# Optimization experiments

Hardware: AMD Instinct MI355X
Metric: run time of the kernel (lower is better)

Reference implementation:

```python
import jax, jax.numpy as jnp
import numpy as np
from jax import lax

B, CIN, H, W = 8, 3, 512, 512
NF, NDOWN, FEAT = 16, 4, 3
NUM_IDS = 32
EPS = 1e-5
DN = ('NCHW', 'OIHW', 'NCHW')


def _inorm(x):
    # torch InstanceNorm2d(affine=False): per-sample per-channel, biased var, eps=1e-5
    m = jnp.mean(x, axis=(2, 3), keepdims=True)
    v = jnp.var(x, axis=(2, 3), keepdims=True)
    return (x - m) * lax.rsqrt(v + EPS)


def _conv(x, w, b, stride=1, pad=0):
    y = lax.conv_general_dilated(x, w, (stride, stride), ((pad, pad), (pad, pad)), dimension_numbers=DN)
    return y + b[None, :, None, None]


def _tconv(x, w, b):
    # torch ConvTranspose2d(k=3, s=2, p=1, output_padding=1); w in torch layout (Cin, Cout, 3, 3)
    wk = jnp.flip(jnp.transpose(w, (1, 0, 2, 3)), axis=(2, 3))  # -> OIHW
    y = lax.conv_general_dilated(x, wk, (1, 1), ((1, 2), (1, 2)), lhs_dilation=(2, 2), dimension_numbers=DN)
    return y + b[None, :, None, None]


def _rpad(x, p):
    return jnp.pad(x, ((0, 0), (0, 0), (p, p), (p, p)), mode='reflect')


def _forward(x, instance_map, w_in, b_in, wd, bd, wu, bu, w_out, b_out):
    h = jax.nn.relu(_inorm(_conv(_rpad(x, 3), w_in, b_in)))
    for w_, b_ in zip(wd, bd):
        h = jax.nn.relu(_inorm(_conv(h, w_, b_, stride=2, pad=1)))
    for w_, b_ in zip(wu, bu):
        h = jax.nn.relu(_inorm(_tconv(h, w_, b_)))
    out = jnp.tanh(_conv(_rpad(h, 3), w_out, b_out))  # [B, FEAT, H, W]
    # per-instance (per-batch, per-channel) mean pooling == fused scatter-mean
    bsz, c, hh, ww = out.shape
    ids = instance_map.reshape(bsz, -1).astype(jnp.int32)     # [B, P]
    f = jnp.transpose(out.reshape(bsz, c, -1), (0, 2, 1))     # [B, P, C]
    seg = lambda ff, ii: jax.ops.segment_sum(ff, ii, num_segments=NUM_IDS)
    sums = jax.vmap(seg)(f, ids)                              # [B, NUM_IDS, C]
    cnt = jax.vmap(seg)(jnp.ones(ids.shape + (1,), f.dtype), ids)  # [B, NUM_IDS, 1]
    means = sums / jnp.maximum(cnt, 1.0)
    pool = jax.vmap(lambda m, ii: m[ii])(means, ids)          # [B, P, C]
    return jnp.transpose(pool, (0, 2, 1)).reshape(bsz, c, hh, ww)


def setup_inputs():
    key = jax.random.key(0)
    ks = jax.random.split(key, 12)
    std = 0.02
    inp = {}
    inp['x'] = jax.random.normal(ks[0], (B, CIN, H, W), jnp.float32)
    inp['instance_map'] = jax.random.randint(ks[1], (B, 1, H, W), 0, NUM_IDS)
    inp['w_in'] = jax.random.normal(ks[2], (NF, CIN, 7, 7), jnp.float32) * std
    inp['b_in'] = jnp.zeros((NF,), jnp.float32)
    for i in range(NDOWN):
        cin = NF * 2 ** i
        inp['w_d%d' % i] = jax.random.normal(ks[3 + i], (2 * cin, cin, 3, 3), jnp.float32) * std
        inp['b_d%d' % i] = jnp.zeros((2 * cin,), jnp.float32)
    for i in range(NDOWN):
        cin = NF * 2 ** (NDOWN - i)
        inp['w_u%d' % i] = jax.random.normal(ks[7 + i], (cin, cin // 2, 3, 3), jnp.float32) * std
        inp['b_u%d' % i] = jnp.zeros((cin // 2,), jnp.float32)
    inp['w_out'] = jax.random.normal(ks[11], (FEAT, NF, 7, 7), jnp.float32) * std
    inp['b_out'] = jnp.zeros((FEAT,), jnp.float32)
    return inp


def reference(x, instance_map, w_in, b_in, w_d0, b_d0, w_d1, b_d1, w_d2, b_d2, w_d3, b_d3, w_u0, b_u0, w_u1, b_u1, w_u2, b_u2, w_u3, b_u3, w_out, b_out):
    wd = [w_d0, w_d1, w_d2, w_d3]
    bd = [b_d0, b_d1, b_d2, b_d3]
    wu = [w_u0, w_u1, w_u2, w_u3]
    bu = [b_u0, b_u1, b_u2, b_u3]
    return _forward(x, instance_map, w_in, b_in, wd, bd, wu, bu, w_out, b_out)
```

## Files before the change

kernel.cpp:

```cpp
#include <hip/hip_runtime.h>
#include <math.h>
#include <type_traits>

#define BATCH 8
#define EPS 1e-5f

__device__ __forceinline__ int refl(int p, int n){ return p<0 ? -p : (p>=n ? 2*n-2-p : p); }


__global__ __launch_bounds__(256) void conv7_in_t(const float* __restrict__ in,
    const float* __restrict__ w, const float* __restrict__ bias, float* __restrict__ out,
    float* __restrict__ statOut){
  const int H=512, W=512;
  __shared__ __align__(16) float wsm[3*49*16];
  __shared__ float bsm[16];
  __shared__ __align__(16) float tile[10][264];
  __shared__ float red[4][32];
  for (int t=threadIdx.x; t<2352; t+=256){
    int j = t & 15; int r = t >> 4;
    wsm[t] = w[j*147 + r];
  }
  if (threadIdx.x < 16) bsm[threadIdx.x] = bias[threadIdx.x];

  int bid = blockIdx.x;
  int b  = bid >> 8;
  int yt = (bid >> 1) & 127;  int y0 = yt*4;
  int xh = bid & 1;           int xbase = xh*256;
  int xq = threadIdx.x & 63;  int ty = threadIdx.x >> 6;
  int x0 = xq*4;              int y  = y0 + ty;

  int gy[10];
  #pragma unroll
  for (int r=0;r<10;r++) gy[r] = refl(y0-3+r, H);

  __syncthreads();
  float acc[16][4];
  #pragma unroll
  for (int j=0;j<16;j++){ float bv=bsm[j];
    #pragma unroll
    for (int p=0;p<4;p++) acc[j][p]=bv; }

  const float* inb = in + (size_t)b*3*H*W;
  for (int ci=0; ci<3; ++ci){
    const float* ipc = inb + (size_t)ci*H*W;
    for (int u=threadIdx.x; u<700; u+=256){
      if (u < 640){
        int r = u >> 6, k = u & 63;
        float4 v = *(const float4*)(ipc + (size_t)gy[r]*W + xbase + 4*k);
        *(float4*)&tile[r][4*k+4] = v;
      } else {
        int u2 = u - 640;
        int r = u2 / 6, h = u2 % 6;
        int L = (h<3) ? (1+h) : (257+h);
        int g = xbase + ((h<3) ? (h-3) : (253+h));
        tile[r][L] = ipc[(size_t)gy[r]*W + refl(g, W)];
      }
    }
    __syncthreads();
    #pragma unroll
    for (int ky=0; ky<7; ++ky){
      const float* tr = &tile[ty+ky][x0];
      float4 A  = *(const float4*)(tr);
      float4 Bv = *(const float4*)(tr+4);
      float4 Cv = *(const float4*)(tr+8);
      float rv[10] = {A.y,A.z,A.w,Bv.x,Bv.y,Bv.z,Bv.w,Cv.x,Cv.y,Cv.z};
      #pragma unroll
      for (int kx=0; kx<7; ++kx){
        const float4* wp = (const float4*)&wsm[(ci*49+ky*7+kx)*16];
        float4 w0=wp[0], w1=wp[1], w2=wp[2], w3=wp[3];
        float wv[16] = {w0.x,w0.y,w0.z,w0.w, w1.x,w1.y,w1.z,w1.w,
                        w2.x,w2.y,w2.z,w2.w, w3.x,w3.y,w3.z,w3.w};
        #pragma unroll
        for (int p=0;p<4;p++){
          float iv = rv[kx+p];
          #pragma unroll
          for (int j=0;j<16;j++) acc[j][p] = fmaf(iv, wv[j], acc[j][p]);
        }
      }
    }
    __syncthreads();
  }

  float* ob = out + ((size_t)(b*16)*H + y)*W + xbase + x0;
  #pragma unroll
  for (int j=0;j<16;j++){
    float4 v = {acc[j][0],acc[j][1],acc[j][2],acc[j][3]};
    *(float4*)(ob + (size_t)j*H*W) = v;
  }
  float ss[16], qq[16];
  #pragma unroll
  for (int j=0;j<16;j++){
    float a=0.f,c=0.f;
    #pragma unroll
    for (int p=0;p<4;p++){ a+=acc[j][p]; c=fmaf(acc[j][p],acc[j][p],c); }
    ss[j]=a; qq[j]=c;
  }
  #pragma unroll
  for (int o=32;o>0;o>>=1){
    #pragma unroll
    for (int j=0;j<16;j++){ ss[j]+=__shfl_down(ss[j],o); qq[j]+=__shfl_down(qq[j],o); }
  }
  int lane = threadIdx.x & 63, wid = threadIdx.x >> 6;
  if (lane==0){
    #pragma unroll
    for (int j=0;j<16;j++){ red[wid][j]=ss[j]; red[wid][16+j]=qq[j]; }
  }
  __syncthreads();
  if (threadIdx.x < 16){
    int j = threadIdx.x;
    float a = red[0][j]+red[1][j]+red[2][j]+red[3][j];
    float c = red[0][16+j]+red[1][16+j]+red[2][16+j]+red[3][16+j];
    float* sp = &statOut[((size_t)b*16 + j)*2];
    atomicAdd(sp, a); atomicAdd(sp+1, c);
  }
}

__global__ __launch_bounds__(256) void conv7_out_t(const float* __restrict__ in,
    const float* __restrict__ w, const float* __restrict__ bias, float* __restrict__ out,
    const float* __restrict__ statIn, const int* __restrict__ imap,
    float* __restrict__ sums, float* __restrict__ cnts){
  const int H=512, W=512;
  __shared__ __align__(16) float wsm[16*49*3];
  __shared__ float bsm[3];
  __shared__ float msm[16], ism[16];
  __shared__ __align__(16) float tile[10][264];
  __shared__ float ls[96];
  __shared__ float lc[32];
  for (int t=threadIdx.x; t<2352; t+=256){
    int j = t % 3; int r = t / 3;
    wsm[t] = w[j*784 + r];
  }
  if (threadIdx.x < 3) bsm[threadIdx.x] = bias[threadIdx.x];
  if (threadIdx.x < 96) ls[threadIdx.x] = 0.f;
  if (threadIdx.x >= 96 && threadIdx.x < 128) lc[threadIdx.x-96] = 0.f;

  int bid = blockIdx.x;
  int b  = bid >> 8;
  int yt = (bid >> 1) & 127;  int y0 = yt*4;
  int xh = bid & 1;           int xbase = xh*256;
  int xq = threadIdx.x & 63;  int ty = threadIdx.x >> 6;
  int x0 = xq*4;              int y  = y0 + ty;

  if (threadIdx.x < 16){
    const float invHW = 1.f/(512.f*512.f);
    float s  = statIn[((size_t)b*16 + threadIdx.x)*2];
    float s2 = statIn[((size_t)b*16 + threadIdx.x)*2+1];
    float m = s*invHW;
    float v = fmaxf(s2*invHW - m*m, 0.f);
    msm[threadIdx.x] = m; ism[threadIdx.x] = rsqrtf(v + EPS);
  }

  int gy[10];
  #pragma unroll
  for (int r=0;r<10;r++) gy[r] = refl(y0-3+r, H);

  __syncthreads();
  float acc[3][4];
  #pragma unroll
  for (int j=0;j<3;j++){ float bv=bsm[j];
    #pragma unroll
    for (int p=0;p<4;p++) acc[j][p]=bv; }

  const float* inb = in + (size_t)b*16*H*W;
  for (int ci=0; ci<16; ++ci){
    const float* ipc = inb + (size_t)ci*H*W;
    float m = msm[ci], is = ism[ci];
    for (int u=threadIdx.x; u<700; u+=256){
      if (u < 640){
        int r = u >> 6, k = u & 63;
        float4 v = *(const float4*)(ipc + (size_t)gy[r]*W + xbase + 4*k);
        v.x = fmaxf((v.x-m)*is, 0.f);
        v.y = fmaxf((v.y-m)*is, 0.f);
        v.z = fmaxf((v.z-m)*is, 0.f);
        v.w = fmaxf((v.w-m)*is, 0.f);
        *(float4*)&tile[r][4*k+4] = v;
      } else {
        int u2 = u - 640;
        int r = u2 / 6, h = u2 % 6;
        int L = (h<3) ? (1+h) : (257+h);
        int g = xbase + ((h<3) ? (h-3) : (253+h));
        float v = ipc[(size_t)gy[r]*W + refl(g, W)];
        tile[r][L] = fmaxf((v-m)*is, 0.f);
      }
    }
    __syncthreads();
    #pragma unroll
    for (int ky=0; ky<7; ++ky){
      const float* tr = &tile[ty+ky][x0];
      float4 A  = *(const float4*)(tr);
      float4 Bv = *(const float4*)(tr+4);
      float4 Cv = *(const float4*)(tr+8);
      float rv[10] = {A.y,A.z,A.w,Bv.x,Bv.y,Bv.z,Bv.w,Cv.x,Cv.y,Cv.z};
      #pragma unroll
      for (int kx=0; kx<7; ++kx){
        const float* wp = &wsm[(ci*49+ky*7+kx)*3];
        float w0=wp[0], w1=wp[1], w2=wp[2];
        #pragma unroll
        for (int p=0;p<4;p++){
          float iv = rv[kx+p];
          acc[0][p] = fmaf(iv, w0, acc[0][p]);
          acc[1][p] = fmaf(iv, w1, acc[1][p]);
          acc[2][p] = fmaf(iv, w2, acc[2][p]);
        }
      }
    }
    __syncthreads();
  }

  #pragma unroll
  for (int j=0;j<3;j++)
    #pragma unroll
    for (int p=0;p<4;p++) acc[j][p] = tanhf(acc[j][p]);

  float* ob = out + ((size_t)(b*3)*H + y)*W + xbase + x0;
  #pragma unroll
  for (int j=0;j<3;j++){
    float4 v0 = {acc[j][0],acc[j][1],acc[j][2],acc[j][3]};
    *(float4*)(ob + (size_t)j*H*W) = v0;
  }

  const int* mb = imap + ((size_t)b*H + y)*W + xbase + x0;
  int4 i0 = *(const int4*)(mb);
  int im[4] = {i0.x,i0.y,i0.z,i0.w};
  #pragma unroll
  for (int p=0;p<4;p++){
    int id = im[p];
    atomicAdd(&ls[id*3+0], acc[0][p]);
    atomicAdd(&ls[id*3+1], acc[1][p]);
    atomicAdd(&ls[id*3+2], acc[2][p]);
    atomicAdd(&lc[id], 1.0f);
  }
  __syncthreads();
  if (threadIdx.x < 96) atomicAdd(&sums[b*96+threadIdx.x], ls[threadIdx.x]);
  if (threadIdx.x >= 96 && threadIdx.x < 128) atomicAdd(&cnts[b*32+threadIdx.x-96], lc[threadIdx.x-96]);
}

template<int CIN, int COT>
__global__ __launch_bounds__(256,4) void conv3s2_lds(const float* __restrict__ in,
    const float* __restrict__ w, const float* __restrict__ bias, float* __restrict__ out,
    int Hin, int Win, const float* __restrict__ statIn, float* __restrict__ statOut){
  const int Cout = 2*CIN;
  const int CG = Cout/COT;
  const int TSTR = 72;
  __shared__ float msm[CIN], ism[CIN];
  __shared__ __align__(16) float tile[2][33*TSTR];
  __shared__ float red[4][2*COT];
  int Hout = Hin>>1, Wout = Win>>1;
  int xtn = Wout>>5, ytn = Hout>>4;
  int bid = blockIdx.x;
  int cgi = bid % CG; int t = bid / CG;
  int xt  = t % xtn;  t /= xtn;
  int yt  = t % ytn;  int b = t / ytn;
  int co0 = cgi*COT;
  int X0 = xt<<5, Y0 = yt<<4;
  int IY0 = 2*Y0-1, GX = X0<<1;
  {
    float invHW = 1.f/(float)(Hin*Win);
    for (int t2=threadIdx.x; t2<CIN; t2+=256){
      float s  = statIn[((size_t)b*CIN + t2)*2];
      float s2 = statIn[((size_t)b*CIN + t2)*2+1];
      float m = s*invHW;
      float v = fmaxf(s2*invHW - m*m, 0.f);
      msm[t2] = m; ism[t2] = rsqrtf(v + EPS);
    }
  }
  __syncthreads();
  const float* inb = in + (size_t)b*CIN*Hin*Win;
  int xx = threadIdx.x & 31, ys = threadIdx.x >> 5;

  float4 vv[3]; float hh[3];
  auto ld = [&](int ci){
    const float* ip = inb + (size_t)ci*Hin*Win;
    float m = msm[ci], is = ism[ci];
    #pragma unroll
    for (int q=0;q<3;q++){
      int u = threadIdx.x + q*256;
      if (u < 561){
        int r = u/17, k = u - r*17;
        int iy = IY0 + r;
        bool okY = (unsigned)iy < (unsigned)Hin;
        if (k < 16){
          float4 v = {0.f,0.f,0.f,0.f};
          if (okY){
            v = *(const float4*)(ip + (size_t)iy*Win + GX + 4*k);
            v.x = fmaxf((v.x-m)*is, 0.f);
            v.y = fmaxf((v.y-m)*is, 0.f);
            v.z = fmaxf((v.z-m)*is, 0.f);
            v.w = fmaxf((v.w-m)*is, 0.f);
          }
          vv[q] = v;
        } else {
          float hv = 0.f;
          if (okY && X0 > 0) hv = fmaxf((ip[(size_t)iy*Win + GX-1]-m)*is, 0.f);
          hh[q] = hv;
        }
      }
    }
  };
  auto st = [&](int buf){
    float* tb = tile[buf];
    #pragma unroll
    for (int q=0;q<3;q++){
      int u = threadIdx.x + q*256;
      if (u < 561){
        int r = u/17, k = u - r*17;
        if (k < 16) *(float4*)(tb + r*TSTR + 4 + 4*k) = vv[q];
        else tb[r*TSTR + 3] = hh[q];
      }
    }
  };

  float acc[COT][2];
  #pragma unroll
  for (int j=0;j<COT;j++){ float bv = bias[co0+j]; acc[j][0]=bv; acc[j][1]=bv; }

  ld(0); st(0);
  for (int ci=0; ci<CIN; ++ci){
    __syncthreads();
    if (ci+1 < CIN) ld(ci+1);
    {
      const float* tb = tile[ci&1];
      float rv[2][3][3];
      #pragma unroll
      for (int g=0;g<2;g++){
        int rb = (ys + (g<<3))<<1;
        #pragma unroll
        for (int ky=0;ky<3;ky++){
          const float* tr = tb + (rb+ky)*TSTR + 3 + (xx<<1);
          rv[g][ky][0]=tr[0]; rv[g][ky][1]=tr[1]; rv[g][ky][2]=tr[2];
        }
      }
      #pragma unroll
      for (int j=0;j<COT;j++){
        const float* wj = w + ((size_t)(co0+j)*CIN + ci)*9;
        float wk[9];
        #pragma unroll
        for (int k=0;k<9;k++) wk[k] = wj[k];
        #pragma unroll
        for (int g=0;g<2;g++)
          #pragma unroll
          for (int ky=0;ky<3;ky++)
            #pragma unroll
            for (int kx=0;kx<3;kx++)
              acc[j][g] = fmaf(rv[g][ky][kx], wk[ky*3+kx], acc[j][g]);
      }
    }
    if (ci+1 < CIN) st((ci+1)&1);
  }

  float* ob = out + ((size_t)b*Cout + co0)*Hout*Wout;
  #pragma unroll
  for (int j=0;j<COT;j++)
    #pragma unroll
    for (int g=0;g<2;g++){
      int oy = ys + (g<<3);
      ob[(size_t)j*Hout*Wout + (Y0+oy)*Wout + X0 + xx] = acc[j][g];
    }
  float ss[COT], qq[COT];
  #pragma unroll
  for (int j=0;j<COT;j++){
    float a = acc[j][0] + acc[j][1];
    float c = fmaf(acc[j][0],acc[j][0], acc[j][1]*acc[j][1]);
    ss[j]=a; qq[j]=c;
  }
  #pragma unroll
  for (int o=32;o>0;o>>=1){
    #pragma unroll
    for (int j=0;j<COT;j++){ ss[j]+=__shfl_down(ss[j],o); qq[j]+=__shfl_down(qq[j],o); }
  }
  int lane = threadIdx.x & 63, wid = threadIdx.x >> 6;
  if (lane==0){
    #pragma unroll
    for (int j=0;j<COT;j++){ red[wid][j]=ss[j]; red[wid][COT+j]=qq[j]; }
  }
  __syncthreads();
  if (threadIdx.x < COT){
    int j = threadIdx.x;
    float a = red[0][j]+red[1][j]+red[2][j]+red[3][j];
    float c = red[0][COT+j]+red[1][COT+j]+red[2][COT+j]+red[3][COT+j];
    float* sp = &statOut[((size_t)b*Cout + co0 + j)*2];
    atomicAdd(sp, a); atomicAdd(sp+1, c);
  }
}

template<int CIN, int COT>
__global__ __launch_bounds__(256,4) void tconv3_lds(const float* __restrict__ in,
    const float* __restrict__ w, const float* __restrict__ bias, float* __restrict__ out,
    int Hin, int Win, const float* __restrict__ statIn, float* __restrict__ statOut){
  const int Cout = CIN/2;
  const int CG = Cout/COT;
  const int TSTR = 36;
  __shared__ float msm[CIN], ism[CIN];
  __shared__ __align__(16) float tile[2][17*TSTR];
  __shared__ float red[4][2*COT];
  int Hout = Hin<<1, Wout = Win<<1;
  int xtn = Win>>5, ytn = Hin>>4;
  int bid = blockIdx.x;
  int cgi = bid % CG; int t = bid / CG;
  int xt  = t % xtn;  t /= xtn;
  int yt  = t % ytn;  int b = t / ytn;
  int co0 = cgi*COT;
  int X0 = xt<<5, Y0 = yt<<4;
  {
    float invHW = 1.f/(float)(Hin*Win);
    for (int t2=threadIdx.x; t2<CIN; t2+=256){
      float s  = statIn[((size_t)b*CIN + t2)*2];
      float s2 = statIn[((size_t)b*CIN + t2)*2+1];
      float m = s*invHW;
      float v = fmaxf(s2*invHW - m*m, 0.f);
      msm[t2] = m; ism[t2] = rsqrtf(v + EPS);
    }
  }
  __syncthreads();
  const float* inb = in + (size_t)b*CIN*Hin*Win;
  int xx = threadIdx.x & 31, ys = threadIdx.x >> 5;

  float4 sv; float sh;
  auto ld = [&](int ci){
    const float* ip = inb + (size_t)ci*Hin*Win;
    float m = msm[ci], is = ism[ci];
    int u = threadIdx.x;
    if (u < 153){
      int r = u/9, k = u - r*9;
      int iy = Y0 + r;
      bool okY = iy < Hin;
      if (k < 8){
        float4 v = {0.f,0.f,0.f,0.f};
        if (okY){
          v = *(const float4*)(ip + (size_t)iy*Win + X0 + 4*k);
          v.x = fmaxf((v.x-m)*is, 0.f);
          v.y = fmaxf((v.y-m)*is, 0.f);
          v.z = fmaxf((v.z-m)*is, 0.f);
          v.w = fmaxf((v.w-m)*is, 0.f);
        }
        sv = v;
      } else {
        float hv = 0.f;
        int xc = X0 + 32;
        if (okY && xc < Win) hv = fmaxf((ip[(size_t)iy*Win + xc]-m)*is, 0.f);
        sh = hv;
      }
    }
  };
  auto st = [&](int buf){
    int u = threadIdx.x;
    if (u < 153){
      int r = u/9, k = u - r*9;
      if (k < 8) *(float4*)(tile[buf] + r*TSTR + 4*k) = sv;
      else tile[buf][r*TSTR + 32] = sh;
    }
  };

  float acc[COT][2][2][2];
  #pragma unroll
  for (int j=0;j<COT;j++){ float bv = bias[co0+j];
    #pragma unroll
    for (int g=0;g<2;g++)
      #pragma unroll
      for (int oy=0;oy<2;oy++){ acc[j][g][oy][0]=bv; acc[j][g][oy][1]=bv; } }

  ld(0); st(0);
  for (int ci=0; ci<CIN; ++ci){
    __syncthreads();
    if (ci+1 < CIN) ld(ci+1);
    {
      const float* tb = tile[ci&1];
      float v[2][2][2];
      #pragma unroll
      for (int g=0;g<2;g++){
        int rb = ys + (g<<3);
        const float* t0 = tb + rb*TSTR + xx;
        v[g][0][0]=t0[0]; v[g][0][1]=t0[1];
        v[g][1][0]=t0[TSTR]; v[g][1][1]=t0[TSTR+1];
      }
      #pragma unroll
      for (int j=0;j<COT;j++){
        const float* wj = w + ((size_t)ci*Cout + co0+j)*9;
        float wk[9];
        #pragma unroll
        for (int k=0;k<9;k++) wk[k] = wj[k];
        #pragma unroll
        for (int g=0;g<2;g++){
          float v00=v[g][0][0], v01=v[g][0][1], v10=v[g][1][0], v11=v[g][1][1];
          acc[j][g][0][0] = fmaf(v00, wk[4], acc[j][g][0][0]);
          acc[j][g][0][1] = fmaf(v00, wk[5], fmaf(v01, wk[3], acc[j][g][0][1]));
          acc[j][g][1][0] = fmaf(v00, wk[7], fmaf(v10, wk[1], acc[j][g][1][0]));
          acc[j][g][1][1] = fmaf(v00, wk[8], fmaf(v01, wk[6],
                             fmaf(v10, wk[2], fmaf(v11, wk[0], acc[j][g][1][1]))));
        }
      }
    }
    if (ci+1 < CIN) st((ci+1)&1);
  }

  float* ob = out + ((size_t)b*Cout + co0)*Hout*Wout;
  #pragma unroll
  for (int j=0;j<COT;j++)
    #pragma unroll
    for (int g=0;g<2;g++)
      #pragma unroll
      for (int oy=0;oy<2;oy++){
        int orow = 2*(Y0 + ys + (g<<3)) + oy;
        float2 v2 = {acc[j][g][oy][0], acc[j][g][oy][1]};
        *(float2*)(ob + (size_t)j*Hout*Wout + (size_t)orow*Wout + 2*(X0+xx)) = v2;
      }
  float ss[COT], qq[COT];
  #pragma unroll
  for (int j=0;j<COT;j++){
    float a=0.f,c=0.f;
    #pragma unroll
    for (int g=0;g<2;g++)
      #pragma unroll
      for (int oy=0;oy<2;oy++)
        #pragma unroll
        for (int ox=0;ox<2;ox++){ float u=acc[j][g][oy][ox]; a+=u; c=fmaf(u,u,c); }
    ss[j]=a; qq[j]=c;
  }
  #pragma unroll
  for (int o=32;o>0;o>>=1){
    #pragma unroll
    for (int j=0;j<COT;j++){ ss[j]+=__shfl_down(ss[j],o); qq[j]+=__shfl_down(qq[j],o); }
  }
  int lane = threadIdx.x & 63, wid = threadIdx.x >> 6;
  if (lane==0){
    #pragma unroll
    for (int j=0;j<COT;j++){ red[wid][j]=ss[j]; red[wid][COT+j]=qq[j]; }
  }
  __syncthreads();
  if (threadIdx.x < COT){
    int j = threadIdx.x;
    float a = red[0][j]+red[1][j]+red[2][j]+red[3][j];
    float c = red[0][COT+j]+red[1][COT+j]+red[2][COT+j]+red[3][COT+j];
    float* sp = &statOut[((size_t)b*Cout + co0 + j)*2];
    atomicAdd(sp, a); atomicAdd(sp+1, c);
  }
}

__global__ void pool_bcast(float* __restrict__ out, const int* __restrict__ imap,
                           const float* __restrict__ sums, const float* __restrict__ cnts){
  const int P = 512*512;
  int b = blockIdx.y;
  __shared__ float lm[96];
  if (threadIdx.x < 96){
    int id = threadIdx.x/3;
    lm[threadIdx.x] = sums[b*96+threadIdx.x] / fmaxf(cnts[b*32+id], 1.0f);
  }
  __syncthreads();
  const int* mb = imap + (size_t)b*P;
  float* ob = out + (size_t)b*3*P;
  for (int p = blockIdx.x*blockDim.x + threadIdx.x; p < P; p += gridDim.x*blockDim.x){
    int id = mb[p];
    ob[p]     = lm[id*3+0];
    ob[P+p]   = lm[id*3+1];
    ob[2*P+p] = lm[id*3+2];
  }
}

static inline int cdiv(int a, int b){ return (a+b-1)/b; }

extern "C" void kernel_launch(void* const* d_in, const int* in_sizes, int n_in,
                              void* d_out, int out_size, void* d_ws, size_t ws_size,
                              hipStream_t stream) {
  const float* x    = (const float*)d_in[0];
  const int*   imap = (const int*)d_in[1];
  const float* w_in = (const float*)d_in[2];
  const float* b_in = (const float*)d_in[3];
  const float *wd[4], *bd[4], *wu[4], *bu[4];
  for (int i=0;i<4;i++){ wd[i]=(const float*)d_in[4+2*i];  bd[i]=(const float*)d_in[5+2*i]; }
  for (int i=0;i<4;i++){ wu[i]=(const float*)d_in[12+2*i]; bu[i]=(const float*)d_in[13+2*i]; }
  const float* w_out = (const float*)d_in[20];
  const float* b_out = (const float*)d_in[21];
  float* out = (float*)d_out;

  char* ws = (char*)d_ws;
  float* A     = (float*)ws;
  float* Bb    = (float*)(ws + (size_t)134217728);
  float* stats = (float*)(ws + (size_t)134217728 + (size_t)67108864);
  float* stLin = stats;
  float* std0  = stLin + 256;
  float* std1  = std0  + 512;
  float* std2  = std1  + 1024;
  float* std3  = std2  + 2048;
  float* stu0  = std3  + 4096;
  float* stu1  = stu0  + 2048;
  float* stu2  = stu1  + 1024;
  float* stu3  = stu2  + 512;
  float* sums  = stu3  + 256;
  float* cnts  = sums  + 768;
  hipMemsetAsync(stats, 0, (size_t)(11776 + 1024)*sizeof(float), stream);

  conv7_in_t<<<2048, 256, 0, stream>>>(x, w_in, b_in, A, stLin);

  conv3s2_lds<16,8><<<4096, 256, 0, stream>>>(A,  wd[0], bd[0], Bb, 512, 512, stLin, std0);
  conv3s2_lds<32,8><<<2048, 256, 0, stream>>>(Bb, wd[1], bd[1], A,  256, 256, std0, std1);
  conv3s2_lds<64,8><<<1024, 256, 0, stream>>>(A,  wd[2], bd[2], Bb, 128, 128, std1, std2);
  conv3s2_lds<128,4><<<1024, 256, 0, stream>>>(Bb, wd[3], bd[3], A,  64,  64, std2, std3);

  tconv3_lds<256,2><<<1024, 256, 0, stream>>>(A,  wu[0], bu[0], Bb, 32, 32, std3, stu0);
  tconv3_lds<128,4><<<1024, 256, 0, stream>>>(Bb, wu[1], bu[1], A,  64, 64, stu0, stu1);
  tconv3_lds<64,4><<<2048, 256, 0, stream>>>(A,  wu[2], bu[2], Bb, 128, 128, stu1, stu2);
  tconv3_lds<32,4><<<4096, 256, 0, stream>>>(Bb, wu[3], bu[3], A,  256, 256, stu2, stu3);

  conv7_out_t<<<2048, 256, 0, stream>>>(A, w_out, b_out, out, stu3, imap, sums, cnts);

  pool_bcast<<<dim3(128,BATCH),256,0,stream>>>(out, imap, sums, cnts);
}
```

Measured before the change: 1.793 ms.

## Compute two output rows per thread in final 7x7 conv, read weights from global

The final 7x7 conv kernel now gives each thread two output rows instead of one, with 8-row tiles per block and half as many blocks. Each loaded tile row feeds both output rows, which reduces halo loads and LDS reads per output. Weights are no longer staged in shared memory. They are loaded directly from global (uniform, likely scalar/cached) into a double-buffered register array. This costs more registers and fewer blocks in flight.

```diff
diff --git a/kernel.cpp b/kernel.cpp
--- a/kernel.cpp
+++ b/kernel.cpp
@@ -120,53 +120,51 @@
     const float* __restrict__ statIn, const int* __restrict__ imap,
     float* __restrict__ sums, float* __restrict__ cnts){
   const int H=512, W=512;
-  __shared__ __align__(16) float wsm[16*49*3];
-  __shared__ float bsm[3];
   __shared__ float msm[16], ism[16];
-  __shared__ __align__(16) float tile[10][264];
+  __shared__ __align__(16) float tile[14][264];
   __shared__ float ls[96];
   __shared__ float lc[32];
-  for (int t=threadIdx.x; t<2352; t+=256){
-    int j = t % 3; int r = t / 3;
-    wsm[t] = w[j*784 + r];
-  }
-  if (threadIdx.x < 3) bsm[threadIdx.x] = bias[threadIdx.x];
   if (threadIdx.x < 96) ls[threadIdx.x] = 0.f;
   if (threadIdx.x >= 96 && threadIdx.x < 128) lc[threadIdx.x-96] = 0.f;
-
-  int bid = blockIdx.x;
-  int b  = bid >> 8;
-  int yt = (bid >> 1) & 127;  int y0 = yt*4;
-  int xh = bid & 1;           int xbase = xh*256;
-  int xq = threadIdx.x & 63;  int ty = threadIdx.x >> 6;
-  int x0 = xq*4;              int y  = y0 + ty;
-
   if (threadIdx.x < 16){
     const float invHW = 1.f/(512.f*512.f);
-    float s  = statIn[((size_t)b*16 + threadIdx.x)*2];
-    float s2 = statIn[((size_t)b*16 + threadIdx.x)*2+1];
+    float s  = statIn[((size_t)blockIdx.x>>7)*32 + threadIdx.x*2];
+    float s2 = statIn[((size_t)blockIdx.x>>7)*32 + threadIdx.x*2+1];
     float m = s*invHW;
     float v = fmaxf(s2*invHW - m*m, 0.f);
     msm[threadIdx.x] = m; ism[threadIdx.x] = rsqrtf(v + EPS);
   }
 
-  int gy[10];
-  #pragma unroll
-  for (int r=0;r<10;r++) gy[r] = refl(y0-3+r, H);
-
-  __syncthreads();
-  float acc[3][4];
-  #pragma unroll
-  for (int j=0;j<3;j++){ float bv=bsm[j];
-    #pragma unroll
-    for (int p=0;p<4;p++) acc[j][p]=bv; }
+  int bid = blockIdx.x;
+  int b  = bid >> 7;
+  int yt = (bid >> 1) & 63;   int y0 = yt*8;
+  int xh = bid & 1;           int xbase = xh*256;
+  int xq = threadIdx.x & 63;  int wid = threadIdx.x >> 6;
+  int x0 = xq*4;
+  int rbase = 2*wid;
+
+  int gy[14];
+  #pragma unroll
+  for (int r=0;r<14;r++) gy[r] = refl(y0-3+r, H);
+
+  __syncthreads();
+  float acc[3][2][4];
+  #pragma unroll
+  for (int j=0;j<3;j++){ float bv = bias[j];
+    #pragma unroll
+    for (int oy=0;oy<2;oy++)
+      #pragma unroll
+      for (int p=0;p<4;p++) acc[j][oy][p]=bv; }
 
   const float* inb = in + (size_t)b*16*H*W;
+  float wbuf[2][21];
   for (int ci=0; ci<16; ++ci){
     const float* ipc = inb + (size_t)ci*H*W;
     float m = msm[ci], is = ism[ci];
-    for (int u=threadIdx.x; u<700; u+=256){
-      if (u < 640){
+    #pragma unroll
+    for (int q=0;q<4;q++){
+      int u = threadIdx.x + q*256;
+      if (u < 896){
         int r = u >> 6, k = u & 63;
         float4 v = *(const float4*)(ipc + (size_t)gy[r]*W + xbase + 4*k);
         v.x = fmaxf((v.x-m)*is, 0.f);
@@ -174,8 +172,8 @@
         v.z = fmaxf((v.z-m)*is, 0.f);
         v.w = fmaxf((v.w-m)*is, 0.f);
         *(float4*)&tile[r][4*k+4] = v;
-      } else {
-        int u2 = u - 640;
+      } else if (u < 980){
+        int u2 = u - 896;
         int r = u2 / 6, h = u2 % 6;
         int L = (h<3) ? (1+h) : (257+h);
         int g = xbase + ((h<3) ? (h-3) : (253+h));
@@ -185,22 +183,44 @@
     }
     __syncthreads();
     #pragma unroll
-    for (int ky=0; ky<7; ++ky){
-      const float* tr = &tile[ty+ky][x0];
+    for (int s=0;s<8;++s){
+      const float* tr = &tile[rbase+s][x0];
       float4 A  = *(const float4*)(tr);
       float4 Bv = *(const float4*)(tr+4);
       float4 Cv = *(const float4*)(tr+8);
       float rv[10] = {A.y,A.z,A.w,Bv.x,Bv.y,Bv.z,Bv.w,Cv.x,Cv.y,Cv.z};
-      #pragma unroll
-      for (int kx=0; kx<7; ++kx){
-        const float* wp = &wsm[(ci*49+ky*7+kx)*3];
-        float w0=wp[0], w1=wp[1], w2=wp[2];
-        #pragma unroll
-        for (int p=0;p<4;p++){
-          float iv = rv[kx+p];
-          acc[0][p] = fmaf(iv, w0, acc[0][p]);
-          acc[1][p] = fmaf(iv, w1, acc[1][p]);
-          acc[2][p] = fmaf(iv, w2, acc[2][p]);
+      if (s < 7){
+        #pragma unroll
+        for (int j=0;j<3;j++){
+          const float* wj = w + j*784 + ci*49 + s*7;
+          #pragma unroll
+          for (int kx=0;kx<7;kx++) wbuf[s&1][kx*3+j] = wj[kx];
+        }
+      }
+      if (s >= 1){
+        #pragma unroll
+        for (int kx=0;kx<7;kx++){
+          float w0=wbuf[(s-1)&1][kx*3], w1=wbuf[(s-1)&1][kx*3+1], w2=wbuf[(s-1)&1][kx*3+2];
+          #pragma unroll
+          for (int p=0;p<4;p++){
+            float iv = rv[kx+p];
+            acc[0][1][p] = fmaf(iv, w0, acc[0][1][p]);
+            acc[1][1][p] = fmaf(iv, w1, acc[1][1][p]);
+            acc[2][1][p] = fmaf(iv, w2, acc[2][1][p]);
+          }
+        }
+      }
+      if (s < 7){
+        #pragma unroll
+        for (int kx=0;kx<7;kx++){
+          float w0=wbuf[s&1][kx*3], w1=wbuf[s&1][kx*3+1], w2=wbuf[s&1][kx*3+2];
+          #pragma unroll
+          for (int p=0;p<4;p++){
+            float iv = rv[kx+p];
+            acc[0][0][p] = fmaf(iv, w0, acc[0][0][p]);
+            acc[1][0][p] = fmaf(iv, w1, acc[1][0][p]);
+            acc[2][0][p] = fmaf(iv, w2, acc[2][0][p]);
+          }
         }
       }
     }
@@ -210,25 +230,35 @@
   #pragma unroll
   for (int j=0;j<3;j++)
     #pragma unroll
-    for (int p=0;p<4;p++) acc[j][p] = tanhf(acc[j][p]);
-
-  float* ob = out + ((size_t)(b*3)*H + y)*W + xbase + x0;
-  #pragma unroll
-  for (int j=0;j<3;j++){
-    float4 v0 = {acc[j][0],acc[j][1],acc[j][2],acc[j][3]};
-    *(float4*)(ob + (size_t)j*H*W) = v0;
-  }
-
-  const int* mb = imap + ((size_t)b*H + y)*W + xbase + x0;
-  int4 i0 = *(const int4*)(mb);
-  int im[4] = {i0.x,i0.y,i0.z,i0.w};
-  #pragma unroll
-  for (int p=0;p<4;p++){
-    int id = im[p];
-    atomicAdd(&ls[id*3+0], acc[0][p]);
-    atomicAdd(&ls[id*3+1], acc[1][p]);
-    atomicAdd(&ls[id*3+2], acc[2][p]);
-    atomicAdd(&lc[id], 1.0f);
+    for (int oy=0;oy<2;oy++)
+      #pragma unroll
+      for (int p=0;p<4;p++) acc[j][oy][p] = tanhf(acc[j][oy][p]);
+
+  #pragma unroll
+  for (int oy=0;oy<2;oy++){
+    int y = y0 + rbase + oy;
+    float* ob = out + ((size_t)(b*3)*H + y)*W + xbase + x0;
+    #pragma unroll
+    for (int j=0;j<3;j++){
+      float4 v0 = {acc[j][oy][0],acc[j][oy][1],acc[j][oy][2],acc[j][oy][3]};
+      *(float4*)(ob + (size_t)j*H*W) = v0;
+    }
+  }
+
+  #pragma unroll
+  for (int oy=0;oy<2;oy++){
+    int y = y0 + rbase + oy;
+    const int* mb = imap + ((size_t)b*H + y)*W + xbase + x0;
+    int4 i0 = *(const int4*)(mb);
+    int im[4] = {i0.x,i0.y,i0.z,i0.w};
+    #pragma unroll
+    for (int p=0;p<4;p++){
+      int id = im[p];
+      atomicAdd(&ls[id*3+0], acc[0][oy][p]);
+      atomicAdd(&ls[id*3+1], acc[1][oy][p]);
+      atomicAdd(&ls[id*3+2], acc[2][oy][p]);
+      atomicAdd(&lc[id], 1.0f);
+    }
   }
   __syncthreads();
   if (threadIdx.x < 96) atomicAdd(&sums[b*96+threadIdx.x], ls[threadIdx.x]);
@@ -601,7 +631,7 @@
   tconv3_lds<64,4><<<2048, 256, 0, stream>>>(A,  wu[2], bu[2], Bb, 128, 128, stu1, stu2);
   tconv3_lds<32,4><<<4096, 256, 0, stream>>>(Bb, wu[3], bu[3], A,  256, 256, stu2, stu3);
 
-  conv7_out_t<<<2048, 256, 0, stream>>>(A, w_out, b_out, out, stu3, imap, sums, cnts);
+  conv7_out_t<<<1024, 256, 0, stream>>>(A, w_out, b_out, out, stu3, imap, sums, cnts);
 
   pool_bcast<<<dim3(128,BATCH),256,0,stream>>>(out, imap, sums, cnts);
 }
```

Result: faster. 1.709 ms (-4.7%).
